# Optimization experiments

Hardware: AMD Instinct MI355X
Metric: run time of the kernel (lower is better)

The kernel has to match this reference:

```python
import jax, jax.numpy as jnp
import numpy as np

UNITS = 512
MEM = 16384
IN_DIM = 512
BATCH = 64
USAGE_DECAY = 0.95


def _hard_sigmoid(x):
    # keras hard_sigmoid: clip(0.2*x + 0.5, 0, 1)
    return jnp.clip(0.2 * x + 0.5, 0.0, 1.0)


def _l2norm(x, axis):
    # K.l2_normalize with eps guard
    return x * jax.lax.rsqrt(jnp.maximum(jnp.sum(x * x, axis=axis, keepdims=True), 1e-12))


def setup_inputs() -> dict:
    key = jax.random.key(0)
    ks = jax.random.split(key, 10)
    bias = jnp.concatenate([
        jnp.zeros((UNITS,), jnp.float32),
        jnp.ones((UNITS,), jnp.float32),   # unit_forget_bias
        jnp.zeros((2 * UNITS,), jnp.float32),
    ])
    return {
        "inputs": jax.random.normal(ks[0], (BATCH, IN_DIM), jnp.float32),
        "h_tm1": jax.random.normal(ks[1], (BATCH, UNITS), jnp.float32) * 0.1,
        "c_tm1": jax.random.normal(ks[2], (BATCH, UNITS), jnp.float32) * 0.1,
        "r_tm1": jax.random.normal(ks[3], (BATCH, UNITS), jnp.float32) * 0.1,
        "m_tm1": jax.random.normal(ks[4], (MEM, UNITS), jnp.float32),
        "c_wu_tm1": jax.random.uniform(ks[5], (MEM, BATCH), jnp.float32),
        "c_wlu_tm1": jax.random.uniform(ks[6], (MEM, BATCH), jnp.float32),
        "c_wr_tm1": jax.random.uniform(ks[7], (MEM, BATCH), jnp.float32),
        "kernel": jax.random.normal(ks[8], (IN_DIM, 4 * UNITS), jnp.float32) * 0.02,
        "recurrent_kernel": jax.random.normal(ks[9], (UNITS, 5 * UNITS), jnp.float32) * 0.02,
        "bias": bias,
        "write_gate": jnp.zeros((1,), jnp.float32),
    }


def reference(inputs, h_tm1, c_tm1, r_tm1, m_tm1, c_wu_tm1, c_wlu_tm1, c_wr_tm1,
              kernel, recurrent_kernel, bias, write_gate):
    u = UNITS
    # --- LSTM gates (no dropout / inference path) ---
    x = inputs @ kernel + bias                         # (B, 4U)
    x_i, x_f, x_c, x_o = jnp.split(x, 4, axis=-1)
    hk = h_tm1 @ recurrent_kernel[:, :4 * u]           # (B, 4U)
    h_i, h_f, h_c, h_o = jnp.split(hk, 4, axis=-1)
    r_i = r_tm1 @ recurrent_kernel[:, 4 * u:]          # read vector feeds input gate
    i_g = _hard_sigmoid(x_i + h_i + r_i)
    f_g = _hard_sigmoid(x_f + h_f)
    c = f_g * c_tm1 + i_g * jnp.tanh(x_c + h_c)
    o_g = _hard_sigmoid(x_o + h_o)
    h = o_g * jnp.tanh(c)                              # (B, U)

    # --- external memory addressing ---
    key_list = h.T                                     # (U, B)
    wg = jax.nn.sigmoid(write_gate)                    # (1,)
    # faithful to source: additive c_wlu_tm1 term (no multiply)
    c_ww = wg * c_wr_tm1 + (1.0 - wg) + c_wlu_tm1      # (M, B)
    n_key = _l2norm(key_list, 0)                       # (U, B)
    n_mem = _l2norm(m_tm1, 1)                          # (M, U)
    cos = n_mem @ n_key                                # (M, B)
    # faithful: K.softmax default axis=-1 => softmax over batch axis
    c_wr = jax.nn.softmax(cos, axis=-1)                # (M, B)
    read = (m_tm1.T @ c_wr).T                          # (B, U)
    c_wu = USAGE_DECAY * c_wu_tm1 + c_wr + c_ww        # (M, B)

    # least-used slot per batch column (top_k with k=M, take last => min)
    nth_smallest = jnp.min(c_wu, axis=0)               # (B,)
    nth_smallest_i = jnp.argmin(c_wu, axis=0)          # (B,)
    c_wlu = (c_wu <= nth_smallest[None, :]).astype(jnp.float32)  # (M, B)

    # zero the least-used rows, then write keys weighted by c_ww
    keep = jnp.prod(1.0 - jax.nn.one_hot(nth_smallest_i, MEM, dtype=jnp.float32), axis=0)  # (M,)
    m = m_tm1 * keep[:, None] + c_ww @ h               # (M, U)

    return h, c, read, m, c_wu, c_wlu, c_wr
```

## Files before the change

### kernel.cpp

```cpp
#include <hip/hip_runtime.h>
#include <math.h>

#define OUT_H    0
#define OUT_C    32768
#define OUT_READ 65536
#define OUT_M    98304
#define OUT_CWU  8486912
#define OUT_CWLU 9535488
#define OUT_CWR  10584064

#define WS_NKF   0
#define WS_HBF   16384
#define WS_PMIN  32768
#define WS_PIDX  49152
#define WS_MINF  65536
#define WS_IDXF  65600
#define WS_RPART 65664

typedef short bf16x8 __attribute__((ext_vector_type(8)));
typedef float f32x4  __attribute__((ext_vector_type(4)));

__device__ __forceinline__ float hsig(float x) {
    return fminf(fmaxf(0.2f * x + 0.5f, 0.f), 1.f);
}
__device__ __forceinline__ unsigned short f2bf(float x) {
    unsigned u = __float_as_uint(x);
    return (unsigned short)((u + 0x7fffu + ((u >> 16) & 1u)) >> 16);
}

__global__ __launch_bounds__(256) void k_preact(
    const float* __restrict__ inputs, const float* __restrict__ h_tm1,
    const float* __restrict__ r_tm1, const float* __restrict__ wk,
    const float* __restrict__ rk, float* __restrict__ pre)
{
    __shared__ alignas(16) float Ast[32][68];
    __shared__ alignas(16) float Bs[32][72];
    const int cb = blockIdx.x % 72, kh = blockIdx.x / 72;
    const int vcol0 = cb * 64;
    const float* A; const float* W; int wstride, wcol0;
    if (vcol0 < 2048)      { A = inputs; W = wk; wstride = 2048; wcol0 = vcol0; }
    else if (vcol0 < 4096) { A = h_tm1;  W = rk; wstride = 2560; wcol0 = vcol0 - 2048; }
    else                   { A = r_tm1;  W = rk; wstride = 2560; wcol0 = 2048 + (vcol0 - 4096); }
    const int tid = threadIdx.x;
    const int rgrp = tid >> 4, cgrp = tid & 15;
    const int srow = tid >> 2, sk = (tid & 3) * 4;
    const int skk = tid >> 3, sc = (tid & 7) * 4;
    float acc[4][4] = {};
    for (int t = 0; t < 4; ++t) {
        const int k0 = kh * 128 + t * 32;
        float4 a0 = *(const float4*)&A[srow * 512 + k0 + sk];
        float4 a1 = *(const float4*)&A[srow * 512 + k0 + 16 + sk];
        float4 w0 = *(const float4*)&W[(size_t)(k0 + skk) * wstride + wcol0 + sc];
        float4 w1 = *(const float4*)&W[(size_t)(k0 + skk) * wstride + wcol0 + 32 + sc];
        Ast[sk + 0][srow] = a0.x; Ast[sk + 1][srow] = a0.y;
        Ast[sk + 2][srow] = a0.z; Ast[sk + 3][srow] = a0.w;
        Ast[16 + sk + 0][srow] = a1.x; Ast[16 + sk + 1][srow] = a1.y;
        Ast[16 + sk + 2][srow] = a1.z; Ast[16 + sk + 3][srow] = a1.w;
        Bs[skk][sc + 0] = w0.x; Bs[skk][sc + 1] = w0.y;
        Bs[skk][sc + 2] = w0.z; Bs[skk][sc + 3] = w0.w;
        Bs[skk][32 + sc + 0] = w1.x; Bs[skk][32 + sc + 1] = w1.y;
        Bs[skk][32 + sc + 2] = w1.z; Bs[skk][32 + sc + 3] = w1.w;
        __syncthreads();
        #pragma unroll
        for (int kk = 0; kk < 32; ++kk) {
            float4 av = *(const float4*)&Ast[kk][rgrp * 4];
            float4 bv = *(const float4*)&Bs[kk][cgrp * 4];
            acc[0][0] += av.x * bv.x; acc[0][1] += av.x * bv.y; acc[0][2] += av.x * bv.z; acc[0][3] += av.x * bv.w;
            acc[1][0] += av.y * bv.x; acc[1][1] += av.y * bv.y; acc[1][2] += av.y * bv.z; acc[1][3] += av.y * bv.w;
            acc[2][0] += av.z * bv.x; acc[2][1] += av.z * bv.y; acc[2][2] += av.z * bv.z; acc[2][3] += av.z * bv.w;
            acc[3][0] += av.w * bv.x; acc[3][1] += av.w * bv.y; acc[3][2] += av.w * bv.z; acc[3][3] += av.w * bv.w;
        }
        __syncthreads();
    }
    float* dst = pre + (size_t)kh * 294912;
    #pragma unroll
    for (int i = 0; i < 4; ++i) {
        float4 v = { acc[i][0], acc[i][1], acc[i][2], acc[i][3] };
        *(float4*)&dst[(rgrp * 4 + i) * 4608 + vcol0 + cgrp * 4] = v;
    }
}

__global__ __launch_bounds__(256) void k_gates(
    const float* __restrict__ pre, const float* __restrict__ bias,
    const float* __restrict__ c_tm1, float* __restrict__ out,
    unsigned short* __restrict__ nkf, unsigned short* __restrict__ hbf)
{
    int b = blockIdx.x, t = threadIdx.x;
    const float* p0 = pre + b * 4608;
    const float* p1 = pre + 294912 + b * 4608;
    const float* p2 = pre + 2 * 294912 + b * 4608;
    const float* p3 = pre + 3 * 294912 + b * 4608;
    float hh[2], cc[2];
    #pragma unroll
    for (int q = 0; q < 2; ++q) {
        int u = t + q * 256;
        #define S4(o) (p0[o] + p1[o] + p2[o] + p3[o])
        float xi = S4(u)        + bias[u];
        float xf = S4(512 + u)  + bias[512 + u];
        float xc = S4(1024 + u) + bias[1024 + u];
        float xo = S4(1536 + u) + bias[1536 + u];
        float hi = S4(2048 + u);
        float hf = S4(2560 + u);
        float hc = S4(3072 + u);
        float ho = S4(3584 + u);
        float ri = S4(4096 + u);
        #undef S4
        float ig = hsig(xi + hi + ri);
        float fg = hsig(xf + hf);
        cc[q] = fg * c_tm1[b * 512 + u] + ig * tanhf(xc + hc);
        float og = hsig(xo + ho);
        hh[q] = og * tanhf(cc[q]);
        out[OUT_H + b * 512 + u] = hh[q];
        out[OUT_C + b * 512 + u] = cc[q];
    }
    float ss = hh[0] * hh[0] + hh[1] * hh[1];
    __shared__ float red[4];
    for (int m = 1; m < 64; m <<= 1) ss += __shfl_xor(ss, m);
    if ((t & 63) == 0) red[t >> 6] = ss;
    __syncthreads();
    float tot = red[0] + red[1] + red[2] + red[3];
    float rn = rsqrtf(fmaxf(tot, 1e-12f));
    #pragma unroll
    for (int q = 0; q < 2; ++q) {
        int u = t + q * 256;
        int s = u >> 5, n = b >> 4;
        int lane = (b & 15) + 16 * ((u & 31) >> 3);
        int e = u & 7;
        nkf[(((s * 4 + n) * 64 + lane) << 3) + e] = f2bf(hh[q] * rn);
        int s2 = b >> 5, N = u >> 4;
        int l2 = (u & 15) + 16 * ((b & 31) >> 3);
        int e2 = b & 7;
        hbf[(((s2 * 32 + N) * 64 + l2) << 3) + e2] = f2bf(hh[q]);
    }
}

__global__ __launch_bounds__(256) void k_cos(
    const float* __restrict__ m_tm1, const unsigned short* __restrict__ nkf,
    const float* __restrict__ cwr_tm1, const float* __restrict__ cwlu_tm1,
    const float* __restrict__ cwu_tm1, const float* __restrict__ wgp,
    float* out, float* __restrict__ pmin, int* __restrict__ pidx)
{
    __shared__ alignas(16) unsigned short Af[2048 * 8];
    __shared__ float rn0[64], rn1[64];
    __shared__ float pmv[4][64];
    __shared__ int   pmi[4][64];
    const int row0 = blockIdx.x * 64;
    const int tid = threadIdx.x;
    const int w = tid >> 6, lane = tid & 63;
    f32x4 acc[4] = {};

    for (int half = 0; half < 2; ++half) {
        for (int i = 0; i < 8; ++i) {
            int r = i * 8 + (tid >> 5);
            int koct = tid & 31;
            const float* src = &m_tm1[(size_t)(row0 + r) * 512 + half * 256 + koct * 8];
            float4 x0 = *(const float4*)src;
            float4 x1 = *(const float4*)&src[4];
            float ssi = x0.x*x0.x + x0.y*x0.y + x0.z*x0.z + x0.w*x0.w
                      + x1.x*x1.x + x1.y*x1.y + x1.z*x1.z + x1.w*x1.w;
            ssi += __shfl_xor(ssi, 1); ssi += __shfl_xor(ssi, 2);
            ssi += __shfl_xor(ssi, 4); ssi += __shfl_xor(ssi, 8);
            ssi += __shfl_xor(ssi, 16);
            if ((tid & 31) == 0) { if (half) rn1[r] = ssi; else rn0[r] = ssi; }
            int s_l = koct >> 2, rt = r >> 4;
            int ln = ((r & 15) + ((koct & 3) << 4)) ^ (s_l & 7);
            union { unsigned short hx[8]; uint4 v; } pk;
            pk.hx[0] = f2bf(x0.x); pk.hx[1] = f2bf(x0.y);
            pk.hx[2] = f2bf(x0.z); pk.hx[3] = f2bf(x0.w);
            pk.hx[4] = f2bf(x1.x); pk.hx[5] = f2bf(x1.y);
            pk.hx[6] = f2bf(x1.z); pk.hx[7] = f2bf(x1.w);
            *(uint4*)&Af[((s_l * 4 + rt) * 64 + ln) << 3] = pk.v;
        }
        __syncthreads();
        for (int s_l = 0; s_l < 8; ++s_l) {
            int lnx = lane ^ (s_l & 7);
            bf16x8 af = *(const bf16x8*)&Af[((s_l * 4 + w) * 64 + lnx) << 3];
            int s = half * 8 + s_l;
            #pragma unroll
            for (int n = 0; n < 4; ++n) {
                bf16x8 bf = *(const bf16x8*)&nkf[((s * 4 + n) * 64 + lane) << 3];
                acc[n] = __builtin_amdgcn_mfma_f32_16x16x32_bf16(af, bf, acc[n], 0, 0, 0);
            }
        }
        __syncthreads();
    }

    const float wg = 1.f / (1.f + expf(-wgp[0]));
    const int lhi = lane >> 4, llo = lane & 15;
    float rsq[4];
    #pragma unroll
    for (int reg = 0; reg < 4; ++reg) {
        int rl = w * 16 + lhi * 4 + reg;
        rsq[reg] = rsqrtf(fmaxf(rn0[rl] + rn1[rl], 1e-12f));
    }
    float bmv[4] = { INFINITY, INFINITY, INFINITY, INFINITY };
    int   bmi[4] = { 0x7fffffff, 0x7fffffff, 0x7fffffff, 0x7fffffff };
    #pragma unroll
    for (int reg = 0; reg < 4; ++reg) {
        int r = row0 + w * 16 + lhi * 4 + reg;
        float c0 = acc[0][reg] * rsq[reg];
        float c1 = acc[1][reg] * rsq[reg];
        float c2 = acc[2][reg] * rsq[reg];
        float c3 = acc[3][reg] * rsq[reg];
        float mx = fmaxf(fmaxf(c0, c1), fmaxf(c2, c3));
        mx = fmaxf(mx, __shfl_xor(mx, 1));
        mx = fmaxf(mx, __shfl_xor(mx, 2));
        mx = fmaxf(mx, __shfl_xor(mx, 4));
        mx = fmaxf(mx, __shfl_xor(mx, 8));
        float e0 = expf(c0 - mx), e1 = expf(c1 - mx);
        float e2 = expf(c2 - mx), e3 = expf(c3 - mx);
        float sm = e0 + e1 + e2 + e3;
        sm += __shfl_xor(sm, 1);
        sm += __shfl_xor(sm, 2);
        sm += __shfl_xor(sm, 4);
        sm += __shfl_xor(sm, 8);
        float inv = 1.f / sm;
        float pv[4] = { e0 * inv, e1 * inv, e2 * inv, e3 * inv };
        #pragma unroll
        for (int n = 0; n < 4; ++n) {
            int g = r * 64 + n * 16 + llo;
            float p = pv[n];
            out[OUT_CWR + g] = p;
            float wr = cwr_tm1[g], wl = cwlu_tm1[g], wu = cwu_tm1[g];
            float cww = wg * wr + (1.f - wg) + wl;
            float cwu = 0.95f * wu + p + cww;
            out[OUT_CWU + g] = cwu;
            if (cwu < bmv[n]) { bmv[n] = cwu; bmi[n] = r; }
        }
    }
    #pragma unroll
    for (int n = 0; n < 4; ++n) {
        #pragma unroll
        for (int mk = 16; mk <= 32; mk <<= 1) {
            float ov = __shfl_xor(bmv[n], mk);
            int   oi = __shfl_xor(bmi[n], mk);
            if (ov < bmv[n] || (ov == bmv[n] && oi < bmi[n])) { bmv[n] = ov; bmi[n] = oi; }
        }
    }
    if (lhi == 0) {
        #pragma unroll
        for (int n = 0; n < 4; ++n) { pmv[w][n * 16 + llo] = bmv[n]; pmi[w][n * 16 + llo] = bmi[n]; }
    }
    __syncthreads();
    if (tid < 64) {
        float bv = pmv[0][tid]; int bi = pmi[0][tid];
        #pragma unroll
        for (int q = 1; q < 4; ++q) {
            float v = pmv[q][tid]; int i2 = pmi[q][tid];
            if (v < bv || (v == bv && i2 < bi)) { bv = v; bi = i2; }
        }
        pmin[blockIdx.x * 64 + tid] = bv;
        pidx[blockIdx.x * 64 + tid] = bi;
    }
}

__global__ __launch_bounds__(256) void k_read_part(
    const float* __restrict__ m_tm1, const float* __restrict__ cwr,
    float* __restrict__ part,
    const float* __restrict__ pmin, const int* __restrict__ pidx,
    float* __restrict__ minf, int* __restrict__ idxf)
{
    __shared__ alignas(16) unsigned short Mf[8192];
    __shared__ alignas(16) unsigned short Cf[8192];
    __shared__ float sv[4]; __shared__ int si[4];
    const int bid = blockIdx.x;
    const int tid = threadIdx.x;
    if (bid < 64) {
        int col = bid;
        float bv = pmin[tid * 64 + col];
        int   bi = pidx[tid * 64 + col];
        for (int mk = 1; mk < 64; mk <<= 1) {
            float ov = __shfl_xor(bv, mk);
            int   oi = __shfl_xor(bi, mk);
            if (ov < bv || (ov == bv && oi < bi)) { bv = ov; bi = oi; }
        }
        if ((tid & 63) == 0) { sv[tid >> 6] = bv; si[tid >> 6] = bi; }
        __syncthreads();
        if (tid == 0) {
            #pragma unroll
            for (int q = 1; q < 4; ++q) {
                if (sv[q] < bv || (sv[q] == bv && si[q] < bi)) { bv = sv[q]; bi = si[q]; }
            }
            minf[col] = bv; idxf[col] = bi;
        }
    }
    const int rs = bid >> 3, us = bid & 7;
    const int row0 = rs * 256, u0 = us * 64;
    const int w = tid >> 6, lane = tid & 63;
    f32x4 acc[4] = {};
    for (int ch = 0; ch < 2; ++ch) {
        const int r0 = row0 + ch * 128;
        __syncthreads();
        #pragma unroll
        for (int q = 0; q < 8; ++q) {
            int idx = q * 1024 + tid * 4;
            int rr = idx >> 6, cc = idx & 63;
            float4 mv = *(const float4*)&m_tm1[(size_t)(r0 + rr) * 512 + u0 + cc];
            float4 cv = *(const float4*)&cwr[(r0 + rr) * 64 + cc];
            int s = rr >> 5, e = rr & 7, lo = 16 * ((rr & 31) >> 3);
            float mvs[4] = { mv.x, mv.y, mv.z, mv.w };
            float cvs[4] = { cv.x, cv.y, cv.z, cv.w };
            #pragma unroll
            for (int i = 0; i < 4; ++i) {
                int col = cc + i;
                int ln = (col & 15) + lo;
                int t4 = col >> 4;
                int slot = (((s * 4 + t4) * 64 + ln) << 3) + e;
                Mf[slot] = f2bf(mvs[i]);
                Cf[slot] = f2bf(cvs[i]);
            }
        }
        __syncthreads();
        #pragma unroll
        for (int s = 0; s < 4; ++s) {
            bf16x8 bf = *(const bf16x8*)&Mf[((s * 4 + w) * 64 + lane) << 3];
            #pragma unroll
            for (int tb = 0; tb < 4; ++tb) {
                bf16x8 af = *(const bf16x8*)&Cf[((s * 4 + tb) * 64 + lane) << 3];
                acc[tb] = __builtin_amdgcn_mfma_f32_16x16x32_bf16(af, bf, acc[tb], 0, 0, 0);
            }
        }
    }
    const int lhi = lane >> 4, llo = lane & 15;
    #pragma unroll
    for (int tb = 0; tb < 4; ++tb) {
        #pragma unroll
        for (int reg = 0; reg < 4; ++reg) {
            int b = tb * 16 + lhi * 4 + reg;
            part[(size_t)rs * 32768 + b * 512 + u0 + w * 16 + llo] = acc[tb][reg];
        }
    }
}

__global__ __launch_bounds__(256) void k_update(
    const float* __restrict__ m_tm1, const float* __restrict__ cwr_tm1,
    const float* __restrict__ cwlu_tm1, const float* __restrict__ wgp,
    const unsigned short* __restrict__ hbf,
    const float* __restrict__ minf, const int* __restrict__ idxf,
    const float* __restrict__ rpart, float* out)
{
    __shared__ float keepf[64];
    __shared__ float minS[64];
    __shared__ int   idxS[64];
    const int rb = blockIdx.x >> 2, us = blockIdx.x & 3;
    const int row0 = rb * 64, u0 = us * 128;
    const int tid = threadIdx.x;
    const int w = tid >> 6, lane = tid & 63;
    const int lhi = lane >> 4, llo = lane & 15;
    if (tid < 64) { idxS[tid] = idxf[tid]; minS[tid] = minf[tid]; }
    __syncthreads();
    if (tid < 64) {
        int gr = row0 + tid;
        float f = 1.f;
        #pragma unroll
        for (int b = 0; b < 64; ++b) if (idxS[b] == gr) f = 0.f;
        keepf[tid] = f;
    }
    __syncthreads();
    const float wg = 1.f / (1.f + expf(-wgp[0]));
    if (us == 0) {
        #pragma unroll
        for (int q = 0; q < 4; ++q) {
            int idx = q * 1024 + tid * 4;
            int r = idx >> 6, b = idx & 63;
            int g = (row0 + r) * 64 + b;
            float4 cu = *(const float4*)&out[OUT_CWU + g];
            float4 res;
            res.x = (cu.x <= minS[b + 0]) ? 1.f : 0.f;
            res.y = (cu.y <= minS[b + 1]) ? 1.f : 0.f;
            res.z = (cu.z <= minS[b + 2]) ? 1.f : 0.f;
            res.w = (cu.w <= minS[b + 3]) ? 1.f : 0.f;
            *(float4*)&out[OUT_CWLU + g] = res;
        }
    } else if (us == 1) {
        if (tid < 128) {
            int gid = rb * 128 + tid;
            float s = 0.f;
            #pragma unroll 8
            for (int rs = 0; rs < 64; ++rs) s += rpart[(size_t)rs * 32768 + gid];
            out[OUT_READ + gid] = s;
        }
    }
    f32x4 acc[8];
    #pragma unroll
    for (int nt = 0; nt < 8; ++nt) {
        #pragma unroll
        for (int reg = 0; reg < 4; ++reg) {
            int rowl = w * 16 + lhi * 4 + reg;
            acc[nt][reg] = m_tm1[(size_t)(row0 + rowl) * 512 + u0 + nt * 16 + llo]
                         * keepf[rowl];
        }
    }
    #pragma unroll
    for (int s = 0; s < 2; ++s) {
        int arow = row0 + w * 16 + llo;
        int base = arow * 64 + s * 32 + lhi * 8;
        float4 c0 = *(const float4*)&cwr_tm1[base];
        float4 c1 = *(const float4*)&cwr_tm1[base + 4];
        float4 l0 = *(const float4*)&cwlu_tm1[base];
        float4 l1 = *(const float4*)&cwlu_tm1[base + 4];
        union { unsigned short hx[8]; bf16x8 v; } af;
        af.hx[0] = f2bf(wg * c0.x + (1.f - wg) + l0.x);
        af.hx[1] = f2bf(wg * c0.y + (1.f - wg) + l0.y);
        af.hx[2] = f2bf(wg * c0.z + (1.f - wg) + l0.z);
        af.hx[3] = f2bf(wg * c0.w + (1.f - wg) + l0.w);
        af.hx[4] = f2bf(wg * c1.x + (1.f - wg) + l1.x);
        af.hx[5] = f2bf(wg * c1.y + (1.f - wg) + l1.y);
        af.hx[6] = f2bf(wg * c1.z + (1.f - wg) + l1.z);
        af.hx[7] = f2bf(wg * c1.w + (1.f - wg) + l1.w);
        #pragma unroll
        for (int nt = 0; nt < 8; ++nt) {
            int N = (u0 >> 4) + nt;
            bf16x8 bf = *(const bf16x8*)&hbf[((s * 32 + N) * 64 + lane) << 3];
            acc[nt] = __builtin_amdgcn_mfma_f32_16x16x32_bf16(af.v, bf, acc[nt], 0, 0, 0);
        }
    }
    #pragma unroll
    for (int nt = 0; nt < 8; ++nt) {
        #pragma unroll
        for (int reg = 0; reg < 4; ++reg) {
            int rowl = w * 16 + lhi * 4 + reg;
            out[OUT_M + (size_t)(row0 + rowl) * 512 + u0 + nt * 16 + llo] = acc[nt][reg];
        }
    }
}

extern "C" void kernel_launch(void* const* d_in, const int* in_sizes, int n_in,
                              void* d_out, int out_size, void* d_ws, size_t ws_size,
                              hipStream_t stream)
{
    const float* inputs    = (const float*)d_in[0];
    const float* h_tm1     = (const float*)d_in[1];
    const float* c_tm1     = (const float*)d_in[2];
    const float* r_tm1     = (const float*)d_in[3];
    const float* m_tm1     = (const float*)d_in[4];
    const float* c_wu_tm1  = (const float*)d_in[5];
    const float* c_wlu_tm1 = (const float*)d_in[6];
    const float* c_wr_tm1  = (const float*)d_in[7];
    const float* wk        = (const float*)d_in[8];
    const float* rk        = (const float*)d_in[9];
    const float* bias      = (const float*)d_in[10];
    const float* wgate     = (const float*)d_in[11];
    float* out = (float*)d_out;
    float* ws  = (float*)d_ws;
    float* pre = out + OUT_M;
    unsigned short* nkf = (unsigned short*)(ws + WS_NKF);
    unsigned short* hbf = (unsigned short*)(ws + WS_HBF);
    float* rpart = ws + WS_RPART;

    k_preact<<<288, 256, 0, stream>>>(inputs, h_tm1, r_tm1, wk, rk, pre);
    k_gates<<<64, 256, 0, stream>>>(pre, bias, c_tm1, out, nkf, hbf);
    k_cos<<<256, 256, 0, stream>>>(m_tm1, nkf, c_wr_tm1, c_wlu_tm1,
                                   c_wu_tm1, wgate, out, ws + WS_PMIN,
                                   (int*)(ws + WS_PIDX));
    k_read_part<<<512, 256, 0, stream>>>(m_tm1, out + OUT_CWR, rpart,
                                         ws + WS_PMIN, (const int*)(ws + WS_PIDX),
                                         ws + WS_MINF, (int*)(ws + WS_IDXF));
    k_update<<<1024, 256, 0, stream>>>(m_tm1, c_wr_tm1, c_wlu_tm1, wgate, hbf,
                                       ws + WS_MINF, (const int*)(ws + WS_IDXF),
                                       rpart, out);
}
```

Measured before the change: 71.56 us.

## Precompute bf16 c_ww fragments in k_cos and reuse them in k_update

k_cos already computes c_ww per element, so it now packs it as bf16 in MFMA fragment layout into shared memory and writes it to a workspace buffer. k_update then loads the ready fragments instead of re-reading c_wr_tm1 and c_wlu_tm1 in fp32 and recomputing the sigmoid and conversions, roughly quartering that input traffic. Separately, the row-norm shuffle reduction in k_cos is deferred until after the loop by accumulating per-thread partial sums, removing shuffles from the load loop. The cost is an extra workspace write from k_cos, reuse of the Af shared buffer after the MFMA loop, and a larger workspace.

```diff
diff --git a/kernel.cpp b/kernel.cpp
--- a/kernel.cpp
+++ b/kernel.cpp
@@ -15,7 +15,8 @@
 #define WS_PIDX  49152
 #define WS_MINF  65536
 #define WS_IDXF  65600
-#define WS_RPART 65664
+#define WS_CWWF  65664
+#define WS_RPART 589952
 
 typedef short bf16x8 __attribute__((ext_vector_type(8)));
 typedef float f32x4  __attribute__((ext_vector_type(4)));
@@ -138,30 +139,29 @@
     const float* __restrict__ m_tm1, const unsigned short* __restrict__ nkf,
     const float* __restrict__ cwr_tm1, const float* __restrict__ cwlu_tm1,
     const float* __restrict__ cwu_tm1, const float* __restrict__ wgp,
-    float* out, float* __restrict__ pmin, int* __restrict__ pidx)
+    float* out, float* __restrict__ pmin, int* __restrict__ pidx,
+    unsigned short* __restrict__ cwwf)
 {
     __shared__ alignas(16) unsigned short Af[2048 * 8];
-    __shared__ float rn0[64], rn1[64];
+    __shared__ float rn[64];
     __shared__ float pmv[4][64];
     __shared__ int   pmi[4][64];
     const int row0 = blockIdx.x * 64;
     const int tid = threadIdx.x;
     const int w = tid >> 6, lane = tid & 63;
     f32x4 acc[4] = {};
+    float ssp[8] = {};
 
     for (int half = 0; half < 2; ++half) {
+        #pragma unroll 2
         for (int i = 0; i < 8; ++i) {
             int r = i * 8 + (tid >> 5);
             int koct = tid & 31;
             const float* src = &m_tm1[(size_t)(row0 + r) * 512 + half * 256 + koct * 8];
             float4 x0 = *(const float4*)src;
             float4 x1 = *(const float4*)&src[4];
-            float ssi = x0.x*x0.x + x0.y*x0.y + x0.z*x0.z + x0.w*x0.w
-                      + x1.x*x1.x + x1.y*x1.y + x1.z*x1.z + x1.w*x1.w;
-            ssi += __shfl_xor(ssi, 1); ssi += __shfl_xor(ssi, 2);
-            ssi += __shfl_xor(ssi, 4); ssi += __shfl_xor(ssi, 8);
-            ssi += __shfl_xor(ssi, 16);
-            if ((tid & 31) == 0) { if (half) rn1[r] = ssi; else rn0[r] = ssi; }
+            ssp[i] += x0.x*x0.x + x0.y*x0.y + x0.z*x0.z + x0.w*x0.w
+                    + x1.x*x1.x + x1.y*x1.y + x1.z*x1.z + x1.w*x1.w;
             int s_l = koct >> 2, rt = r >> 4;
             int ln = ((r & 15) + ((koct & 3) << 4)) ^ (s_l & 7);
             union { unsigned short hx[8]; uint4 v; } pk;
@@ -184,6 +184,15 @@
         }
         __syncthreads();
     }
+    #pragma unroll
+    for (int i = 0; i < 8; ++i) {
+        float v = ssp[i];
+        v += __shfl_xor(v, 1); v += __shfl_xor(v, 2);
+        v += __shfl_xor(v, 4); v += __shfl_xor(v, 8);
+        v += __shfl_xor(v, 16);
+        if ((tid & 31) == 0) rn[i * 8 + (tid >> 5)] = v;
+    }
+    __syncthreads();
 
     const float wg = 1.f / (1.f + expf(-wgp[0]));
     const int lhi = lane >> 4, llo = lane & 15;
@@ -191,7 +200,7 @@
     #pragma unroll
     for (int reg = 0; reg < 4; ++reg) {
         int rl = w * 16 + lhi * 4 + reg;
-        rsq[reg] = rsqrtf(fmaxf(rn0[rl] + rn1[rl], 1e-12f));
+        rsq[reg] = rsqrtf(fmaxf(rn[rl], 1e-12f));
     }
     float bmv[4] = { INFINITY, INFINITY, INFINITY, INFINITY };
     int   bmi[4] = { 0x7fffffff, 0x7fffffff, 0x7fffffff, 0x7fffffff };
@@ -225,6 +234,12 @@
             float cww = wg * wr + (1.f - wg) + wl;
             float cwu = 0.95f * wu + p + cww;
             out[OUT_CWU + g] = cwu;
+            {
+                int rowl16 = lhi * 4 + reg;
+                int s2 = n >> 1;
+                int l2 = rowl16 + 16 * (((n & 1) << 1) + (llo >> 3));
+                Af[(((s2 * 4 + w) * 64 + l2) << 3) + (llo & 7)] = f2bf(cww);
+            }
             if (cwu < bmv[n]) { bmv[n] = cwu; bmi[n] = r; }
         }
     }
@@ -242,6 +257,12 @@
         for (int n = 0; n < 4; ++n) { pmv[w][n * 16 + llo] = bmv[n]; pmi[w][n * 16 + llo] = bmi[n]; }
     }
     __syncthreads();
+    {
+        uint4* dst = (uint4*)&cwwf[(size_t)blockIdx.x * 4096];
+        const uint4* srcp = (const uint4*)Af;
+        dst[tid] = srcp[tid];
+        dst[tid + 256] = srcp[tid + 256];
+    }
     if (tid < 64) {
         float bv = pmv[0][tid]; int bi = pmi[0][tid];
         #pragma unroll
@@ -333,8 +354,7 @@
 }
 
 __global__ __launch_bounds__(256) void k_update(
-    const float* __restrict__ m_tm1, const float* __restrict__ cwr_tm1,
-    const float* __restrict__ cwlu_tm1, const float* __restrict__ wgp,
+    const float* __restrict__ m_tm1, const unsigned short* __restrict__ cwwf,
     const unsigned short* __restrict__ hbf,
     const float* __restrict__ minf, const int* __restrict__ idxf,
     const float* __restrict__ rpart, float* out)
@@ -357,7 +377,6 @@
         keepf[tid] = f;
     }
     __syncthreads();
-    const float wg = 1.f / (1.f + expf(-wgp[0]));
     if (us == 0) {
         #pragma unroll
         for (int q = 0; q < 4; ++q) {
@@ -393,26 +412,12 @@
     }
     #pragma unroll
     for (int s = 0; s < 2; ++s) {
-        int arow = row0 + w * 16 + llo;
-        int base = arow * 64 + s * 32 + lhi * 8;
-        float4 c0 = *(const float4*)&cwr_tm1[base];
-        float4 c1 = *(const float4*)&cwr_tm1[base + 4];
-        float4 l0 = *(const float4*)&cwlu_tm1[base];
-        float4 l1 = *(const float4*)&cwlu_tm1[base + 4];
-        union { unsigned short hx[8]; bf16x8 v; } af;
-        af.hx[0] = f2bf(wg * c0.x + (1.f - wg) + l0.x);
-        af.hx[1] = f2bf(wg * c0.y + (1.f - wg) + l0.y);
-        af.hx[2] = f2bf(wg * c0.z + (1.f - wg) + l0.z);
-        af.hx[3] = f2bf(wg * c0.w + (1.f - wg) + l0.w);
-        af.hx[4] = f2bf(wg * c1.x + (1.f - wg) + l1.x);
-        af.hx[5] = f2bf(wg * c1.y + (1.f - wg) + l1.y);
-        af.hx[6] = f2bf(wg * c1.z + (1.f - wg) + l1.z);
-        af.hx[7] = f2bf(wg * c1.w + (1.f - wg) + l1.w);
+        bf16x8 af = *(const bf16x8*)&cwwf[(size_t)rb * 4096 + (((s * 4 + w) * 64 + lane) << 3)];
         #pragma unroll
         for (int nt = 0; nt < 8; ++nt) {
             int N = (u0 >> 4) + nt;
             bf16x8 bf = *(const bf16x8*)&hbf[((s * 32 + N) * 64 + lane) << 3];
-            acc[nt] = __builtin_amdgcn_mfma_f32_16x16x32_bf16(af.v, bf, acc[nt], 0, 0, 0);
+            acc[nt] = __builtin_amdgcn_mfma_f32_16x16x32_bf16(af, bf, acc[nt], 0, 0, 0);
         }
     }
     #pragma unroll
@@ -444,19 +449,20 @@
     float* out = (float*)d_out;
     float* ws  = (float*)d_ws;
     float* pre = out + OUT_M;
-    unsigned short* nkf = (unsigned short*)(ws + WS_NKF);
-    unsigned short* hbf = (unsigned short*)(ws + WS_HBF);
+    unsigned short* nkf  = (unsigned short*)(ws + WS_NKF);
+    unsigned short* hbf  = (unsigned short*)(ws + WS_HBF);
+    unsigned short* cwwf = (unsigned short*)(ws + WS_CWWF);
     float* rpart = ws + WS_RPART;
 
     k_preact<<<288, 256, 0, stream>>>(inputs, h_tm1, r_tm1, wk, rk, pre);
     k_gates<<<64, 256, 0, stream>>>(pre, bias, c_tm1, out, nkf, hbf);
     k_cos<<<256, 256, 0, stream>>>(m_tm1, nkf, c_wr_tm1, c_wlu_tm1,
                                    c_wu_tm1, wgate, out, ws + WS_PMIN,
-                                   (int*)(ws + WS_PIDX));
+                                   (int*)(ws + WS_PIDX), cwwf);
     k_read_part<<<512, 256, 0, stream>>>(m_tm1, out + OUT_CWR, rpart,
                                          ws + WS_PMIN, (const int*)(ws + WS_PIDX),
                                          ws + WS_MINF, (int*)(ws + WS_IDXF));
-    k_update<<<1024, 256, 0, stream>>>(m_tm1, c_wr_tm1, c_wlu_tm1, wgate, hbf,
+    k_update<<<1024, 256, 0, stream>>>(m_tm1, cwwf, hbf,
                                        ws + WS_MINF, (const int*)(ws + WS_IDXF),
                                        rpart, out);
 }
```

Measured after the change: 66.53 us. 7.0% less time.
